# Kernel optimization log

Hardware: AMD Instinct MI355X
Metric: run time of the kernel (lower is better)

Reference implementation:

```python
import jax, jax.numpy as jnp
import numpy as np

B, S, D, H = 2, 2048, 1024, 16
DK = D // H

def setup_inputs() -> dict:
    key = jax.random.key(0)
    ks = jax.random.split(key, 11)
    scale = 1.0 / np.sqrt(D)
    inp = {
        'query': jax.random.normal(ks[0], (B, S, D), jnp.float32),
        'key':   jax.random.normal(ks[1], (B, S, D), jnp.float32),
        'value': jax.random.normal(ks[2], (B, S, D), jnp.float32),
        'wq': jax.random.normal(ks[3], (D, D), jnp.float32) * scale,
        'bq': jax.random.normal(ks[4], (D,), jnp.float32) * 0.01,
        'wk': jax.random.normal(ks[5], (D, D), jnp.float32) * scale,
        'bk': jax.random.normal(ks[6], (D,), jnp.float32) * 0.01,
        'wv': jax.random.normal(ks[7], (D, D), jnp.float32) * scale,
        'bv': jax.random.normal(ks[8], (D,), jnp.float32) * 0.01,
        'wo': jax.random.normal(ks[9], (D, D), jnp.float32) * scale,
        'bo': jax.random.normal(ks[10], (D,), jnp.float32) * 0.01,
    }
    return inp

def reference(query, key, value, wq, bq, wk, bk, wv, bv, wo, bo):
    nb = query.shape[0]
    # projections: torch nn.Linear computes x @ W^T + b; here weights stored as (in,out)
    def proj(x, w, b):
        return (x @ w + b).reshape(nb, -1, H, DK).transpose(0, 2, 1, 3)  # [B,H,S,dk]
    q = proj(query, wq, bq)
    k = proj(key, wk, bk)
    v = proj(value, wv, bv)
    scores = jnp.einsum('bhqd,bhkd->bhqk', q, k) / jnp.sqrt(jnp.float32(DK))
    p = jax.nn.softmax(scores, axis=-1)  # dropout p=0 (eval)
    x = jnp.einsum('bhqk,bhkd->bhqd', p, v)
    x = x.transpose(0, 2, 1, 3).reshape(nb, -1, H * DK)
    return x @ wo + bo
```

## Files before the change

kernel.cpp:

```cpp
#include <hip/hip_runtime.h>


typedef __attribute__((ext_vector_type(8))) __bf16 bf16x8;
typedef __attribute__((ext_vector_type(4))) __bf16 bf16x4;
typedef __attribute__((ext_vector_type(8))) float f32x8;
typedef __attribute__((ext_vector_type(4))) float f32x4;

#define MFMA16 __builtin_amdgcn_mfma_f32_16x16x32_bf16

union Bf8 { bf16x8 v; __bf16 e[8]; };

__device__ inline f32x4 zero4() { f32x4 z; z[0]=z[1]=z[2]=z[3]=0.f; return z; }

__device__ inline float fast_exp2(float x) {
#if __has_builtin(__builtin_amdgcn_exp2f)
    return __builtin_amdgcn_exp2f(x);
#else
    return __expf(x * 0.6931471805599453f);
#endif
}

__device__ inline void load_lds16(const void* g, void* l) {
    __builtin_amdgcn_global_load_lds(
        (const __attribute__((address_space(1))) unsigned int*)g,
        (__attribute__((address_space(3))) unsigned int*)l, 16, 0, 0);
}

__global__ __launch_bounds__(256) void prep_all(
        const float* __restrict__ w0, const float* __restrict__ w1,
        const float* __restrict__ w2, const float* __restrict__ w3,
        const float* __restrict__ x0, const float* __restrict__ x1,
        const float* __restrict__ x2,
        __bf16* __restrict__ wt, __bf16* __restrict__ d0,
        __bf16* __restrict__ d1, __bf16* __restrict__ d2) {
    const int z = blockIdx.z, t = threadIdx.x;
    if (z < 4) {
        const float* src = z == 0 ? w0 : z == 1 ? w1 : z == 2 ? w2 : w3;
        __bf16* dst = wt + (size_t)z * 1048576;
        __shared__ float tile[32][33];
        const int tc = t & 31, tr = t >> 5;
        const int r0 = blockIdx.y * 32, c0 = blockIdx.x * 32;
#pragma unroll
        for (int i = 0; i < 4; i++) {
            int r = tr + i * 8;
            tile[r][tc] = src[(size_t)(r0 + r) * 1024 + c0 + tc];
        }
        __syncthreads();
#pragma unroll
        for (int i = 0; i < 4; i++) {
            int r = tr + i * 8;
            dst[(size_t)(c0 + r) * 1024 + r0 + tc] = (__bf16)tile[tc][r];
        }
    } else {
        const float* src = z == 4 ? x0 : z == 5 ? x1 : x2;
        __bf16* dst = z == 4 ? d0 : z == 5 ? d1 : d2;
        int bid = blockIdx.y * 32 + blockIdx.x;
        size_t g = ((size_t)bid * 256 + t) * 16;
#pragma unroll
        for (int h = 0; h < 2; h++) {
            f32x8 a = *(const f32x8*)&src[g + h * 8];
            Bf8 tmp;
#pragma unroll
            for (int j = 0; j < 8; j++) tmp.e[j] = (__bf16)a[j];
            *(bf16x8*)&dst[g + h * 8] = tmp.v;
        }
    }
}

template <int MODE, typename OutT>
__device__ inline void gemm_fast_core(__bf16* __restrict__ smem,
                                      const __bf16* __restrict__ A,
                                      const __bf16* __restrict__ Bt,
                                      const float* __restrict__ bias,
                                      OutT* __restrict__ out, float scale) {
    __bf16* As = smem;
    __bf16* Bs = smem + 8192;
    const int t = threadIdx.x;
    const int wave = t >> 6, lane = t & 63, lm = lane & 15, quad = lane >> 4;
    const int m0 = blockIdx.y * 128, n0 = blockIdx.x * 128;
    const int wm = (wave >> 1) * 64, wn = (wave & 1) * 64;

    f32x4 acc[4][4];
#pragma unroll
    for (int i = 0; i < 4; i++)
#pragma unroll
        for (int j = 0; j < 4; j++) acc[i][j] = zero4();

    for (int k0 = 0; k0 < 1024; k0 += 64) {
#pragma unroll
        for (int i = 0; i < 4; i++) {
            int s = i * 256 + t;
            int row = s >> 3, cb = (s & 7) ^ (row & 7);
            size_t goff = (size_t)row * 1024 + k0 + cb * 8;
            load_lds16(&A[(size_t)m0 * 1024 + goff],
                       &As[(size_t)(i * 256 + wave * 64) * 8]);
            load_lds16(&Bt[(size_t)n0 * 1024 + goff],
                       &Bs[(size_t)(i * 256 + wave * 64) * 8]);
        }
        __syncthreads();
#pragma unroll
        for (int ks = 0; ks < 2; ks++) {
            bf16x8 af[4], bfr[4];
#pragma unroll
            for (int mt = 0; mt < 4; mt++)
                af[mt] = *(const bf16x8*)&As[(wm + mt * 16 + lm) * 64 +
                                             (((ks * 4 + quad) ^ (lm & 7)) * 8)];
#pragma unroll
            for (int nt = 0; nt < 4; nt++)
                bfr[nt] = *(const bf16x8*)&Bs[(wn + nt * 16 + lm) * 64 +
                                              (((ks * 4 + quad) ^ (lm & 7)) * 8)];
#pragma unroll
            for (int mt = 0; mt < 4; mt++)
#pragma unroll
                for (int nt = 0; nt < 4; nt++)
                    acc[mt][nt] = MFMA16(af[mt], bfr[nt], acc[mt][nt], 0, 0, 0);
        }
        __syncthreads();
    }

    float bv4[4];
#pragma unroll
    for (int nt = 0; nt < 4; nt++) bv4[nt] = bias[n0 + wn + nt * 16 + lm];

    if (MODE == 2) {
#pragma unroll
        for (int mt = 0; mt < 4; mt++)
#pragma unroll
            for (int r = 0; r < 4; r++) {
                int rr = wm + mt * 16 + quad * 4 + r;
#pragma unroll
                for (int nt = 0; nt < 4; nt++) {
                    int c = wn + nt * 16 + lm;
                    smem[c * 128 + (rr ^ (8 * (c & 15)))] =
                        (__bf16)((acc[mt][nt][r] + bv4[nt]) * scale);
                }
            }
        __syncthreads();
        const int b = m0 >> 11;
#pragma unroll
        for (int it = 0; it < 8; it++) {
            int g = it * 256 + t;
            int c = g >> 4, gr = g & 15;
            bf16x8 v = *(const bf16x8*)&smem[c * 128 + ((gr * 8) ^ (8 * (c & 15)))];
            int col = n0 + c, hh = col >> 6, dk = col & 63;
            int sglob = (m0 & 2047) + gr * 8;
            size_t idx = (size_t)(b * 16 + hh) * 131072 + (size_t)dk * 2048 + sglob;
            *(bf16x8*)&out[idx] = v;
        }
    } else {
#pragma unroll
        for (int mt = 0; mt < 4; mt++) {
#pragma unroll
            for (int r = 0; r < 4; r++) {
                int row = m0 + wm + mt * 16 + quad * 4 + r;
#pragma unroll
                for (int nt = 0; nt < 4; nt++) {
                    int col = n0 + wn + nt * 16 + lm;
                    float val = (acc[mt][nt][r] + bv4[nt]) * scale;
                    size_t idx;
                    if (MODE == 0) {
                        idx = (size_t)row * 1024 + col;
                    } else {
                        int b = row >> 11, s = row & 2047, hh = col >> 6, dk = col & 63;
                        idx = (size_t)(b * 16 + hh) * 131072 + (size_t)s * 64 + dk;
                    }
                    out[idx] = (OutT)val;
                }
            }
        }
    }
}

__global__ __launch_bounds__(256) void proj_fast3(
        const __bf16* __restrict__ xq, const __bf16* __restrict__ xk,
        const __bf16* __restrict__ xv, const __bf16* __restrict__ WT,
        const float* __restrict__ bq, const float* __restrict__ bk,
        const float* __restrict__ bv,
        __bf16* __restrict__ Q, __bf16* __restrict__ K, __bf16* __restrict__ Vt) {
    __shared__ __bf16 smem[16384];
    int z = blockIdx.z;
    if (z == 0)
        gemm_fast_core<1, __bf16>(smem, xq, WT, bq, Q, 0.18033688f);
    else if (z == 1)
        gemm_fast_core<1, __bf16>(smem, xk, WT + 1048576, bk, K, 1.f);
    else
        gemm_fast_core<2, __bf16>(smem, xv, WT + 2097152, bv, Vt, 1.f);
}

__global__ __launch_bounds__(256) void out_proj_fast64(
        const __bf16* __restrict__ A, const __bf16* __restrict__ Bt,
        const float* __restrict__ bias, float* __restrict__ out) {
    __shared__ __bf16 As[8192];
    __shared__ __bf16 Bs[4096];
    const int t = threadIdx.x;
    const int wave = t >> 6, lane = t & 63, lm = lane & 15, quad = lane >> 4;
    const int m0 = blockIdx.y * 128, n0 = blockIdx.x * 64;
    const int wm = (wave >> 1) * 64, wn = (wave & 1) * 32;

    f32x4 acc[4][2];
#pragma unroll
    for (int i = 0; i < 4; i++) { acc[i][0] = zero4(); acc[i][1] = zero4(); }

    for (int k0 = 0; k0 < 1024; k0 += 64) {
#pragma unroll
        for (int i = 0; i < 4; i++) {
            int s = i * 256 + t;
            int row = s >> 3, cb = (s & 7) ^ (row & 7);
            load_lds16(&A[(size_t)(m0 + row) * 1024 + k0 + cb * 8],
                       &As[(size_t)(i * 256 + wave * 64) * 8]);
            if (i < 2)
                load_lds16(&Bt[(size_t)(n0 + row) * 1024 + k0 + cb * 8],
                           &Bs[(size_t)(i * 256 + wave * 64) * 8]);
        }
        __syncthreads();
#pragma unroll
        for (int ks = 0; ks < 2; ks++) {
            bf16x8 af[4], bfr[2];
#pragma unroll
            for (int mt = 0; mt < 4; mt++)
                af[mt] = *(const bf16x8*)&As[(wm + mt * 16 + lm) * 64 +
                                             (((ks * 4 + quad) ^ (lm & 7)) * 8)];
#pragma unroll
            for (int nt = 0; nt < 2; nt++)
                bfr[nt] = *(const bf16x8*)&Bs[(wn + nt * 16 + lm) * 64 +
                                              (((ks * 4 + quad) ^ (lm & 7)) * 8)];
#pragma unroll
            for (int mt = 0; mt < 4; mt++)
#pragma unroll
                for (int nt = 0; nt < 2; nt++)
                    acc[mt][nt] = MFMA16(af[mt], bfr[nt], acc[mt][nt], 0, 0, 0);
        }
        __syncthreads();
    }

    float bv2[2];
#pragma unroll
    for (int nt = 0; nt < 2; nt++) bv2[nt] = bias[n0 + wn + nt * 16 + lm];

#pragma unroll
    for (int mt = 0; mt < 4; mt++)
#pragma unroll
        for (int r = 0; r < 4; r++) {
            int row = m0 + wm + mt * 16 + quad * 4 + r;
#pragma unroll
            for (int nt = 0; nt < 2; nt++) {
                int col = n0 + wn + nt * 16 + lm;
                out[(size_t)row * 1024 + col] = acc[mt][nt][r] + bv2[nt];
            }
        }
}

__global__ __launch_bounds__(256, 2) void attn_kernel(
        const __bf16* __restrict__ Q, const __bf16* __restrict__ K,
        const __bf16* __restrict__ Vt, __bf16* __restrict__ O) {
    __shared__ __bf16 Ks[8192];
    __shared__ __bf16 Vs[8192];
    __shared__ __bf16 Ps[4 * 32 * 136];
    const int t = threadIdx.x;
    const int wave = t >> 6, lane = t & 63, lm = lane & 15, quad = lane >> 4;
    const int q0 = blockIdx.x * 128;
    const int bh = blockIdx.y;
    const size_t base = (size_t)bh * 131072;

    bf16x8 bq[2][2];
    {
        int qrow = q0 + wave * 32;
#pragma unroll
        for (int nt = 0; nt < 2; nt++)
#pragma unroll
            for (int ks = 0; ks < 2; ks++)
                bq[nt][ks] = *(const bf16x8*)
                    &Q[base + (size_t)(qrow + nt * 16 + lm) * 64 + ks * 32 + quad * 8];
    }

    float m_run[2], l_run[2];
#pragma unroll
    for (int n = 0; n < 2; n++) { m_run[n] = -1e30f; l_run[n] = 0.f; }
    f32x4 o_acc[4][2];
#pragma unroll
    for (int mt = 0; mt < 4; mt++)
#pragma unroll
        for (int n = 0; n < 2; n++) o_acc[mt][n] = zero4();

    __bf16* Pw = &Ps[wave * 32 * 136];

    for (int kv0 = 0; kv0 < 2048; kv0 += 128) {
#pragma unroll
        for (int i = 0; i < 4; i++) {
            int s = i * 256 + t;
            {
                int row = s >> 3, cb = (s & 7) ^ (row & 7);
                load_lds16(&K[base + (size_t)(kv0 + row) * 64 + cb * 8],
                           &Ks[(size_t)(i * 256 + wave * 64) * 8]);
            }
            {
                int row = s >> 4, cb = (s & 15) ^ (row & 15);
                load_lds16(&Vt[base + (size_t)row * 2048 + kv0 + cb * 8],
                           &Vs[(size_t)(i * 256 + wave * 64) * 8]);
            }
        }
        __syncthreads();

        f32x4 sc[8][2];
#pragma unroll
        for (int mt = 0; mt < 8; mt++) {
            sc[mt][0] = zero4();
            sc[mt][1] = zero4();
#pragma unroll
            for (int ks = 0; ks < 2; ks++) {
                bf16x8 ak = *(const bf16x8*)&Ks[(mt * 16 + lm) * 64 +
                                                (((ks * 4 + quad) ^ (lm & 7)) * 8)];
                sc[mt][0] = MFMA16(ak, bq[0][ks], sc[mt][0], 0, 0, 0);
                sc[mt][1] = MFMA16(ak, bq[1][ks], sc[mt][1], 0, 0, 0);
            }
        }

#pragma unroll
        for (int nt = 0; nt < 2; nt++) {
            float mx = -1e30f;
#pragma unroll
            for (int mt = 0; mt < 8; mt++)
#pragma unroll
                for (int r = 0; r < 4; r++) mx = fmaxf(mx, sc[mt][nt][r]);
            mx = fmaxf(mx, __shfl_xor(mx, 16));
            mx = fmaxf(mx, __shfl_xor(mx, 32));
            float mn = fmaxf(m_run[nt], mx);
            float alpha = fast_exp2(m_run[nt] - mn);
            m_run[nt] = mn;
            float su = 0.f;
#pragma unroll
            for (int mt = 0; mt < 8; mt++)
#pragma unroll
                for (int r = 0; r < 4; r++) {
                    float p = fast_exp2(sc[mt][nt][r] - mn);
                    sc[mt][nt][r] = p;
                    su += p;
                }
            su += __shfl_xor(su, 16);
            su += __shfl_xor(su, 32);
            l_run[nt] = l_run[nt] * alpha + su;
#pragma unroll
            for (int mt = 0; mt < 4; mt++)
#pragma unroll
                for (int r = 0; r < 4; r++) o_acc[mt][nt][r] *= alpha;
        }

#pragma unroll
        for (int nt = 0; nt < 2; nt++)
#pragma unroll
            for (int mt = 0; mt < 8; mt++) {
                bf16x4 pk;
#pragma unroll
                for (int r = 0; r < 4; r++) pk[r] = (__bf16)sc[mt][nt][r];
                *(bf16x4*)&Pw[(nt * 16 + lm) * 136 + mt * 16 + quad * 4] = pk;
            }
        __asm__ volatile("" ::: "memory");

#pragma unroll
        for (int ks = 0; ks < 4; ks++) {
            bf16x8 bp[2];
#pragma unroll
            for (int nt = 0; nt < 2; nt++)
                bp[nt] = *(const bf16x8*)&Pw[(nt * 16 + lm) * 136 + ks * 32 + quad * 8];
#pragma unroll
            for (int mt = 0; mt < 4; mt++) {
                bf16x8 av = *(const bf16x8*)&Vs[(mt * 16 + lm) * 128 +
                                                (((ks * 4 + quad) ^ lm) * 8)];
                o_acc[mt][0] = MFMA16(av, bp[0], o_acc[mt][0], 0, 0, 0);
                o_acc[mt][1] = MFMA16(av, bp[1], o_acc[mt][1], 0, 0, 0);
            }
        }
        __syncthreads();
    }

#pragma unroll
    for (int nt = 0; nt < 2; nt++) {
        float inv = 1.f / l_run[nt];
#pragma unroll
        for (int mt = 0; mt < 4; mt++) {
            bf16x4 pk;
#pragma unroll
            for (int r = 0; r < 4; r++) pk[r] = (__bf16)(o_acc[mt][nt][r] * inv);
            *(bf16x4*)&Pw[(nt * 16 + lm) * 136 + mt * 16 + quad * 4] = pk;
        }
    }
    __asm__ volatile("" ::: "memory");
    {
        const int b = bh >> 4, h = bh & 15;
        int ql = lane >> 1, half = lane & 1;
        int srow = q0 + wave * 32 + ql;
#pragma unroll
        for (int j = 0; j < 4; j++) {
            bf16x8 v = *(const bf16x8*)&Pw[ql * 136 + half * 32 + j * 8];
            *(bf16x8*)&O[(size_t)(b * 2048 + srow) * 1024 + h * 64 + half * 32 + j * 8] = v;
        }
    }
}

extern "C" void kernel_launch(void* const* d_in, const int* in_sizes, int n_in,
                              void* d_out, int out_size, void* d_ws, size_t ws_size,
                              hipStream_t stream) {
    if (ws_size < ((size_t)40 << 20)) return;

    const float* query = (const float*)d_in[0];
    const float* key_  = (const float*)d_in[1];
    const float* value = (const float*)d_in[2];
    const float* wq = (const float*)d_in[3];
    const float* bq = (const float*)d_in[4];
    const float* wk = (const float*)d_in[5];
    const float* bk = (const float*)d_in[6];
    const float* wv = (const float*)d_in[7];
    const float* bv = (const float*)d_in[8];
    const float* wo = (const float*)d_in[9];
    const float* bo = (const float*)d_in[10];
    float* out = (float*)d_out;

    char* ws = (char*)d_ws;
    __bf16* WT  = (__bf16*)(ws);
    __bf16* Qw  = (__bf16*)(ws + ((size_t)8  << 20));
    __bf16* Kw  = (__bf16*)(ws + ((size_t)16 << 20));
    __bf16* Vtw = (__bf16*)(ws + ((size_t)24 << 20));
    __bf16* Ow  = (__bf16*)(ws + ((size_t)32 << 20));

    __bf16* Xq = Ow;
    __bf16* Xk = (__bf16*)d_out;
    __bf16* Xv = (__bf16*)d_out + 4194304;

    prep_all<<<dim3(32, 32, 7), dim3(256), 0, stream>>>(
        wq, wk, wv, wo, query, key_, value, WT, Xq, Xk, Xv);
    proj_fast3<<<dim3(8, 32, 3), dim3(256), 0, stream>>>(
        Xq, Xk, Xv, WT, bq, bk, bv, Qw, Kw, Vtw);
    attn_kernel<<<dim3(16, 32), dim3(256), 0, stream>>>(Qw, Kw, Vtw, Ow);
    out_proj_fast64<<<dim3(16, 32), dim3(256), 0, stream>>>(
        Ow, WT + 3 * 1048576, bo, out);
}
```

Measured before the change: 236.9 us.

## Double-buffer K/V tiles in attention with smaller KV block and MFMA priority

The attention kernel now splits K/V into 64-wide tiles held in two LDS buffers. The next tile is loaded asynchronously while the current one is computed, so global-to-LDS loads overlap MFMA and softmax work instead of stalling at a barrier each iteration. The P staging buffer shrinks to match the smaller tile, and s_setprio raises wave priority around the MFMA sections. In exchange, the loop runs twice as many iterations, which doubles the barriers and the per-tile softmax rescale overhead.

Result: no change. 240.8 us (+1.7%).

```diff
diff --git a/kernel.cpp b/kernel.cpp
--- a/kernel.cpp
+++ b/kernel.cpp
@@ -253,9 +253,9 @@
 __global__ __launch_bounds__(256, 2) void attn_kernel(
         const __bf16* __restrict__ Q, const __bf16* __restrict__ K,
         const __bf16* __restrict__ Vt, __bf16* __restrict__ O) {
-    __shared__ __bf16 Ks[8192];
-    __shared__ __bf16 Vs[8192];
-    __shared__ __bf16 Ps[4 * 32 * 136];
+    __shared__ __bf16 Ks[2][4096];
+    __shared__ __bf16 Vs[2][4096];
+    __shared__ __bf16 Ps[4 * 32 * 72];
     const int t = threadIdx.x;
     const int wave = t >> 6, lane = t & 63, lm = lane & 15, quad = lane >> 4;
     const int q0 = blockIdx.x * 128;
@@ -282,44 +282,48 @@
 #pragma unroll
         for (int n = 0; n < 2; n++) o_acc[mt][n] = zero4();
 
-    __bf16* Pw = &Ps[wave * 32 * 136];
-
-    for (int kv0 = 0; kv0 < 2048; kv0 += 128) {
-#pragma unroll
-        for (int i = 0; i < 4; i++) {
+    __bf16* Pw = &Ps[wave * 32 * 72];
+
+    auto stage = [&](int buf, int kv0) {
+#pragma unroll
+        for (int i = 0; i < 2; i++) {
             int s = i * 256 + t;
-            {
-                int row = s >> 3, cb = (s & 7) ^ (row & 7);
-                load_lds16(&K[base + (size_t)(kv0 + row) * 64 + cb * 8],
-                           &Ks[(size_t)(i * 256 + wave * 64) * 8]);
-            }
-            {
-                int row = s >> 4, cb = (s & 15) ^ (row & 15);
-                load_lds16(&Vt[base + (size_t)row * 2048 + kv0 + cb * 8],
-                           &Vs[(size_t)(i * 256 + wave * 64) * 8]);
-            }
-        }
-        __syncthreads();
-
-        f32x4 sc[8][2];
-#pragma unroll
-        for (int mt = 0; mt < 8; mt++) {
+            int row = s >> 3, cb = (s & 7) ^ (row & 7);
+            load_lds16(&K[base + (size_t)(kv0 + row) * 64 + cb * 8],
+                       &Ks[buf][(i * 256 + wave * 64) * 8]);
+            load_lds16(&Vt[base + (size_t)row * 2048 + kv0 + cb * 8],
+                       &Vs[buf][(i * 256 + wave * 64) * 8]);
+        }
+    };
+
+    stage(0, 0);
+    __syncthreads();
+
+    for (int it = 0; it < 32; ++it) {
+        const int cur = it & 1;
+        if (it < 31) stage(cur ^ 1, (it + 1) * 64);
+
+        f32x4 sc[4][2];
+        __builtin_amdgcn_s_setprio(1);
+#pragma unroll
+        for (int mt = 0; mt < 4; mt++) {
             sc[mt][0] = zero4();
             sc[mt][1] = zero4();
 #pragma unroll
             for (int ks = 0; ks < 2; ks++) {
-                bf16x8 ak = *(const bf16x8*)&Ks[(mt * 16 + lm) * 64 +
+                bf16x8 ak = *(const bf16x8*)&Ks[cur][(mt * 16 + lm) * 64 +
                                                 (((ks * 4 + quad) ^ (lm & 7)) * 8)];
                 sc[mt][0] = MFMA16(ak, bq[0][ks], sc[mt][0], 0, 0, 0);
                 sc[mt][1] = MFMA16(ak, bq[1][ks], sc[mt][1], 0, 0, 0);
             }
         }
+        __builtin_amdgcn_s_setprio(0);
 
 #pragma unroll
         for (int nt = 0; nt < 2; nt++) {
             float mx = -1e30f;
 #pragma unroll
-            for (int mt = 0; mt < 8; mt++)
+            for (int mt = 0; mt < 4; mt++)
 #pragma unroll
                 for (int r = 0; r < 4; r++) mx = fmaxf(mx, sc[mt][nt][r]);
             mx = fmaxf(mx, __shfl_xor(mx, 16));
@@ -329,7 +333,7 @@
             m_run[nt] = mn;
             float su = 0.f;
 #pragma unroll
-            for (int mt = 0; mt < 8; mt++)
+            for (int mt = 0; mt < 4; mt++)
 #pragma unroll
                 for (int r = 0; r < 4; r++) {
                     float p = fast_exp2(sc[mt][nt][r] - mn);
@@ -348,28 +352,31 @@
 #pragma unroll
         for (int nt = 0; nt < 2; nt++)
 #pragma unroll
-            for (int mt = 0; mt < 8; mt++) {
+            for (int mt = 0; mt < 4; mt++) {
                 bf16x4 pk;
 #pragma unroll
                 for (int r = 0; r < 4; r++) pk[r] = (__bf16)sc[mt][nt][r];
-                *(bf16x4*)&Pw[(nt * 16 + lm) * 136 + mt * 16 + quad * 4] = pk;
+                *(bf16x4*)&Pw[(nt * 16 + lm) * 72 + mt * 16 + quad * 4] = pk;
             }
         __asm__ volatile("" ::: "memory");
 
-#pragma unroll
-        for (int ks = 0; ks < 4; ks++) {
+        __builtin_amdgcn_s_setprio(1);
+#pragma unroll
+        for (int ks = 0; ks < 2; ks++) {
             bf16x8 bp[2];
 #pragma unroll
             for (int nt = 0; nt < 2; nt++)
-                bp[nt] = *(const bf16x8*)&Pw[(nt * 16 + lm) * 136 + ks * 32 + quad * 8];
+                bp[nt] = *(const bf16x8*)&Pw[(nt * 16 + lm) * 72 + ks * 32 + quad * 8];
 #pragma unroll
             for (int mt = 0; mt < 4; mt++) {
-                bf16x8 av = *(const bf16x8*)&Vs[(mt * 16 + lm) * 128 +
-                                                (((ks * 4 + quad) ^ lm) * 8)];
+                bf16x8 av = *(const bf16x8*)&Vs[cur][(mt * 16 + lm) * 64 +
+                                                (((ks * 4 + quad) ^ (lm & 7)) * 8)];
                 o_acc[mt][0] = MFMA16(av, bp[0], o_acc[mt][0], 0, 0, 0);
                 o_acc[mt][1] = MFMA16(av, bp[1], o_acc[mt][1], 0, 0, 0);
             }
         }
+        __builtin_amdgcn_s_setprio(0);
+
         __syncthreads();
     }
 
@@ -381,7 +388,7 @@
             bf16x4 pk;
 #pragma unroll
             for (int r = 0; r < 4; r++) pk[r] = (__bf16)(o_acc[mt][nt][r] * inv);
-            *(bf16x4*)&Pw[(nt * 16 + lm) * 136 + mt * 16 + quad * 4] = pk;
+            *(bf16x4*)&Pw[(nt * 16 + lm) * 72 + mt * 16 + quad * 4] = pk;
         }
     }
     __asm__ volatile("" ::: "memory");
@@ -391,7 +398,7 @@
         int srow = q0 + wave * 32 + ql;
 #pragma unroll
         for (int j = 0; j < 4; j++) {
-            bf16x8 v = *(const bf16x8*)&Pw[ql * 136 + half * 32 + j * 8];
+            bf16x8 v = *(const bf16x8*)&Pw[ql * 72 + half * 32 + j * 8];
             *(bf16x8*)&O[(size_t)(b * 2048 + srow) * 1024 + h * 64 + half * 32 + j * 8] = v;
         }
     }
```
